# Optimization experiments

Measured on AMD Instinct MI355X. Metric: run time of the kernel, lower is better.

## Reference

```python
import jax, jax.numpy as jnp
import numpy as np

N = 8192
RANK_RATIO = 1.0


def setup_inputs() -> dict:
    key = jax.random.key(0)
    k1, k2, k3 = jax.random.split(key, 3)
    logit = jax.random.normal(k1, (N, 1), dtype=jnp.float32)
    status = jax.random.randint(k2, (N,), 0, 2).astype(jnp.float32)  # event indicator in {0,1}
    time = jax.random.uniform(k3, (N,), dtype=jnp.float32) * 10.0    # survival times
    status_time = jnp.stack([status, time], axis=1)  # [N, 2]
    return {"logit": logit, "status_time": status_time}


def reference(logit, status_time):
    status = status_time[:, 0]
    time = status_time[:, 1]
    lg = -logit.squeeze()  # [N]

    # Comparable pair (i, j): time[i] < time[j] and status[i] == 1.
    # i is the 'low' index (shorter, uncensored time), j is the 'high' index.
    mask = (time[:, None] < time[None, :]) & (status[:, None] == 1.0)  # [N, N]
    # rank term: relu(1 - lg[high] + lg[low])^2 over comparable pairs
    hinge = jnp.maximum(1.0 - lg[None, :] + lg[:, None], 0.0)
    sq = hinge * hinge
    n_pairs = jnp.maximum(jnp.sum(mask), 1)  # mean over selected pairs
    rank_loss = jnp.sum(jnp.where(mask, sq, 0.0)) / n_pairs.astype(sq.dtype)

    uncensor_part = time - lg
    censor_part = jnp.maximum(uncensor_part, 0.0)
    reg_term = (1.0 - status) * censor_part + status * uncensor_part
    reg_loss = jnp.mean(reg_term * reg_term)

    return RANK_RATIO * rank_loss + (1.0 - RANK_RATIO) * reg_loss
```

## Files before the change

kernel.cpp:

```cpp
#include <hip/hip_runtime.h>


typedef float f32x2 __attribute__((ext_vector_type(2)));

constexpr int N_   = 8192;
constexpr int BLK  = 256;
constexpr int R    = 4;
constexpr int JPB  = BLK * R;
constexpr int NJB  = N_ / JPB;
constexpr int ICH  = 32;
constexpr int NIC  = N_ / ICH;
constexpr int GRID = NJB * NIC;

__global__ __launch_bounds__(BLK) void svm_partial(
        const float* __restrict__ logit,
        const float* __restrict__ st,
        float* __restrict__ psum,
        int*   __restrict__ pcnt) {
    __shared__ float2 ci_s[ICH];

    const int jb = blockIdx.x & (NJB - 1);
    const int ic = blockIdx.x / NJB;
    const int j0 = jb * JPB + (int)threadIdx.x * R;

    const float4 lj4 = *(const float4*)(logit + j0);
    const float4 sa  = *(const float4*)(st + 2 * j0);
    const float4 sb  = *(const float4*)(st + 2 * j0 + 4);
    const f32x2 nljpA = { -(1.0f + lj4.x), -(1.0f + lj4.y) };
    const f32x2 nljpB = { -(1.0f + lj4.z), -(1.0f + lj4.w) };
    const float tj0 = sa.y, tj1 = sa.w, tj2 = sb.y, tj3 = sb.w;

    const int i0 = ic * ICH;
    if (threadIdx.x < ICH) {
        const int    i  = i0 + (int)threadIdx.x;
        const float  li = logit[i];
        const float2 sv = *(const float2*)(st + 2 * i);
        const float  te = (sv.x == 1.0f) ? sv.y : 1e30f;
        ci_s[threadIdx.x] = make_float2(li, te);
    }
    __syncthreads();

    f32x2 sA = {0.f, 0.f}, sB = {0.f, 0.f};
    int cnt = 0;
    #pragma unroll 8
    for (int k = 0; k < ICH; ++k) {
        const float2 ct = ci_s[k];
        const float  li = ct.x, te = ct.y;
        const f32x2  li2 = { li, li };
        f32x2 xA = li2 + nljpA;
        f32x2 xB = li2 + nljpB;
        float h0 = fminf(xA.x, 0.f);
        float h1 = fminf(xA.y, 0.f);
        float h2 = fminf(xB.x, 0.f);
        float h3 = fminf(xB.y, 0.f);
        const bool m0 = te < tj0;
        const bool m1 = te < tj1;
        const bool m2 = te < tj2;
        const bool m3 = te < tj3;
        f32x2 hmA = { m0 ? h0 : 0.f, m1 ? h1 : 0.f };
        f32x2 hmB = { m2 ? h2 : 0.f, m3 ? h3 : 0.f };
        sA += hmA * hmA;
        sB += hmB * hmB;
        cnt += (int)__popcll(__ballot(m0));
        cnt += (int)__popcll(__ballot(m1));
        cnt += (int)__popcll(__ballot(m2));
        cnt += (int)__popcll(__ballot(m3));
    }

    float sum = (sA.x + sA.y) + (sB.x + sB.y);
    for (int off = 32; off > 0; off >>= 1)
        sum += __shfl_down(sum, off, 64);

    __shared__ float wsum[BLK / 64];
    __shared__ int   wcnt[BLK / 64];
    const int lane = threadIdx.x & 63;
    const int wid  = threadIdx.x >> 6;
    if (lane == 0) { wsum[wid] = sum; wcnt[wid] = cnt; }
    __syncthreads();
    if (threadIdx.x == 0) {
        psum[blockIdx.x] = (wsum[0] + wsum[1]) + (wsum[2] + wsum[3]);
        pcnt[blockIdx.x] =  wcnt[0] + wcnt[1] + wcnt[2] + wcnt[3];
    }
}

__global__ __launch_bounds__(BLK) void svm_final(
        const float* __restrict__ psum,
        const int* __restrict__ pcnt,
        float* __restrict__ out) {
    float s = 0.f;
    int   c = 0;
    for (int t = (int)threadIdx.x; t < GRID; t += BLK) {
        s += psum[t];
        c += pcnt[t];
    }
    for (int off = 32; off > 0; off >>= 1) {
        s += __shfl_down(s, off, 64);
        c += __shfl_down(c, off, 64);
    }
    __shared__ float wsum[BLK / 64];
    __shared__ int   wcnt[BLK / 64];
    const int lane = threadIdx.x & 63;
    const int wid  = threadIdx.x >> 6;
    if (lane == 0) { wsum[wid] = s; wcnt[wid] = c; }
    __syncthreads();
    if (threadIdx.x == 0) {
        const float S = (wsum[0] + wsum[1]) + (wsum[2] + wsum[3]);
        const int   C =  wcnt[0] + wcnt[1] + wcnt[2] + wcnt[3];
        out[0] = S / (float)(C > 0 ? C : 1);
    }
}

extern "C" void kernel_launch(void* const* d_in, const int* in_sizes, int n_in,
                              void* d_out, int out_size, void* d_ws, size_t ws_size,
                              hipStream_t stream) {
    const float* logit = (const float*)d_in[0];
    const float* st    = (const float*)d_in[1];

    float* psum = (float*)d_ws;
    int*   pcnt = (int*)((char*)d_ws + GRID * 4);

    svm_partial<<<GRID, BLK, 0, stream>>>(logit, st, psum, pcnt);
    svm_final<<<1, BLK, 0, stream>>>(psum, pcnt, (float*)d_out);
}
```

Measured before the change: 19.09 us.

## Fuse final reduction into partial kernel via last-block atomic counters

Merges the two-kernel reduction into a single kernel. Each block publishes a packed (sum,count) pair, and the last block of each group of 32, chosen by an atomic counter, reduces that group. The last group then produces the final output. The i-chunk size is doubled to halve the grid. This removes a second kernel launch and its dependency gap, at the cost of atomics and counters that are never reset but rely on modular wraparound across calls.

```diff
diff --git a/kernel.cpp b/kernel.cpp
--- a/kernel.cpp
+++ b/kernel.cpp
@@ -8,19 +8,28 @@
 constexpr int R    = 4;
 constexpr int JPB  = BLK * R;
 constexpr int NJB  = N_ / JPB;
-constexpr int ICH  = 32;
+constexpr int ICH  = 64;
 constexpr int NIC  = N_ / ICH;
 constexpr int GRID = NJB * NIC;
+constexpr int GSZ  = 32;
+constexpr int NGRP = GRID / GSZ;
 
-__global__ __launch_bounds__(BLK) void svm_partial(
+__global__ __launch_bounds__(BLK) void svm_onepass(
         const float* __restrict__ logit,
         const float* __restrict__ st,
-        float* __restrict__ psum,
-        int*   __restrict__ pcnt) {
+        unsigned long long* __restrict__ pair,
+        unsigned long long* __restrict__ gpair,
+        unsigned int* __restrict__ gcnt,
+        unsigned int* __restrict__ fcnt,
+        float* __restrict__ out) {
     __shared__ float2 ci_s[ICH];
+    __shared__ float  wsum[BLK / 64];
+    __shared__ int    wcnt[BLK / 64];
+    __shared__ bool   lastg_s, lastf_s;
 
     const int jb = blockIdx.x & (NJB - 1);
     const int ic = blockIdx.x / NJB;
+    const int g  = blockIdx.x / GSZ;
     const int j0 = jb * JPB + (int)threadIdx.x * R;
 
     const float4 lj4 = *(const float4*)(logit + j0);
@@ -71,42 +80,71 @@
     for (int off = 32; off > 0; off >>= 1)
         sum += __shfl_down(sum, off, 64);
 
-    __shared__ float wsum[BLK / 64];
-    __shared__ int   wcnt[BLK / 64];
     const int lane = threadIdx.x & 63;
     const int wid  = threadIdx.x >> 6;
     if (lane == 0) { wsum[wid] = sum; wcnt[wid] = cnt; }
     __syncthreads();
     if (threadIdx.x == 0) {
-        psum[blockIdx.x] = (wsum[0] + wsum[1]) + (wsum[2] + wsum[3]);
-        pcnt[blockIdx.x] =  wcnt[0] + wcnt[1] + wcnt[2] + wcnt[3];
+        const float s = (wsum[0] + wsum[1]) + (wsum[2] + wsum[3]);
+        const int   c =  wcnt[0] + wcnt[1] + wcnt[2] + wcnt[3];
+        const unsigned long long p =
+            ((unsigned long long)(unsigned int)c << 32) |
+             (unsigned long long)__float_as_uint(s);
+        __hip_atomic_store(&pair[blockIdx.x], p,
+                           __ATOMIC_RELAXED, __HIP_MEMORY_SCOPE_AGENT);
+        const unsigned int old = __hip_atomic_fetch_add(
+            &gcnt[g], 1u, __ATOMIC_ACQ_REL, __HIP_MEMORY_SCOPE_AGENT);
+        lastg_s = ((old + 1u) & (GSZ - 1u)) == 0u;
     }
-}
+    __syncthreads();
+    if (!lastg_s) return;
 
-__global__ __launch_bounds__(BLK) void svm_final(
-        const float* __restrict__ psum,
-        const int* __restrict__ pcnt,
-        float* __restrict__ out) {
-    float s = 0.f;
-    int   c = 0;
-    for (int t = (int)threadIdx.x; t < GRID; t += BLK) {
-        s += psum[t];
-        c += pcnt[t];
+    {
+        float s = 0.f; int c = 0;
+        if (threadIdx.x < GSZ) {
+            const unsigned long long p = __hip_atomic_load(
+                &pair[g * GSZ + threadIdx.x],
+                __ATOMIC_RELAXED, __HIP_MEMORY_SCOPE_AGENT);
+            s = __uint_as_float((unsigned int)p);
+            c = (int)(unsigned int)(p >> 32);
+        }
+        if (threadIdx.x < 64) {
+            for (int off = 16; off > 0; off >>= 1) {
+                s += __shfl_down(s, off, 64);
+                c += __shfl_down(c, off, 64);
+            }
+            if (threadIdx.x == 0) {
+                const unsigned long long p =
+                    ((unsigned long long)(unsigned int)c << 32) |
+                     (unsigned long long)__float_as_uint(s);
+                __hip_atomic_store(&gpair[g], p,
+                                   __ATOMIC_RELAXED, __HIP_MEMORY_SCOPE_AGENT);
+                const unsigned int old2 = __hip_atomic_fetch_add(
+                    fcnt, 1u, __ATOMIC_ACQ_REL, __HIP_MEMORY_SCOPE_AGENT);
+                lastf_s = ((old2 + 1u) & (NGRP - 1u)) == 0u;
+            }
+        }
     }
-    for (int off = 32; off > 0; off >>= 1) {
-        s += __shfl_down(s, off, 64);
-        c += __shfl_down(c, off, 64);
-    }
-    __shared__ float wsum[BLK / 64];
-    __shared__ int   wcnt[BLK / 64];
-    const int lane = threadIdx.x & 63;
-    const int wid  = threadIdx.x >> 6;
-    if (lane == 0) { wsum[wid] = s; wcnt[wid] = c; }
     __syncthreads();
-    if (threadIdx.x == 0) {
-        const float S = (wsum[0] + wsum[1]) + (wsum[2] + wsum[3]);
-        const int   C =  wcnt[0] + wcnt[1] + wcnt[2] + wcnt[3];
-        out[0] = S / (float)(C > 0 ? C : 1);
+    if (!lastf_s) return;
+
+    {
+        float s = 0.f; int c = 0;
+        if (threadIdx.x < NGRP) {
+            const unsigned long long p = __hip_atomic_load(
+                &gpair[threadIdx.x],
+                __ATOMIC_RELAXED, __HIP_MEMORY_SCOPE_AGENT);
+            s = __uint_as_float((unsigned int)p);
+            c = (int)(unsigned int)(p >> 32);
+        }
+        if (threadIdx.x < 64) {
+            for (int off = 16; off > 0; off >>= 1) {
+                s += __shfl_down(s, off, 64);
+                c += __shfl_down(c, off, 64);
+            }
+            if (threadIdx.x == 0)
+                out[0] = s / (float)(c > 0 ? c : 1);
+        }
     }
 }
 
@@ -116,9 +154,11 @@
     const float* logit = (const float*)d_in[0];
     const float* st    = (const float*)d_in[1];
 
-    float* psum = (float*)d_ws;
-    int*   pcnt = (int*)((char*)d_ws + GRID * 4);
+    unsigned long long* pair  = (unsigned long long*)d_ws;
+    unsigned long long* gpair = (unsigned long long*)((char*)d_ws + 8192);
+    unsigned int*       gcnt  = (unsigned int*)((char*)d_ws + 8448);
+    unsigned int*       fcnt  = (unsigned int*)((char*)d_ws + 8576);
 
-    svm_partial<<<GRID, BLK, 0, stream>>>(logit, st, psum, pcnt);
-    svm_final<<<1, BLK, 0, stream>>>(psum, pcnt, (float*)d_out);
+    svm_onepass<<<GRID, BLK, 0, stream>>>(logit, st, pair, gpair, gcnt, fcnt,
+                                          (float*)d_out);
 }
```

Measured after the change: 28.60 us. 49.9% more time.

## Compact uncensored i rows via ballot and count pairs per lane

Applied to the files above, without the earlier changes.

The i-chunk grows to 64, and only rows with status==1 are compacted into shared memory using a wave ballot and prefix popcount. The inner loop then runs over just those rows, which skips about half of the pair work. Per-iteration ballot/popcount counting is replaced by per-lane integer counters reduced once with shuffles. Because the loop trip count is now data-dependent, unrolling is partial, and the larger chunk halves the grid size.

```diff
diff --git a/kernel.cpp b/kernel.cpp
--- a/kernel.cpp
+++ b/kernel.cpp
@@ -8,7 +8,7 @@
 constexpr int R    = 4;
 constexpr int JPB  = BLK * R;
 constexpr int NJB  = N_ / JPB;
-constexpr int ICH  = 32;
+constexpr int ICH  = 64;
 constexpr int NIC  = N_ / ICH;
 constexpr int GRID = NJB * NIC;
 
@@ -18,6 +18,7 @@
         float* __restrict__ psum,
         int*   __restrict__ pcnt) {
     __shared__ float2 ci_s[ICH];
+    __shared__ int    total_s;
 
     const int jb = blockIdx.x & (NJB - 1);
     const int ic = blockIdx.x / NJB;
@@ -30,20 +31,23 @@
     const f32x2 nljpB = { -(1.0f + lj4.z), -(1.0f + lj4.w) };
     const float tj0 = sa.y, tj1 = sa.w, tj2 = sb.y, tj3 = sb.w;
 
-    const int i0 = ic * ICH;
-    if (threadIdx.x < ICH) {
-        const int    i  = i0 + (int)threadIdx.x;
-        const float  li = logit[i];
-        const float2 sv = *(const float2*)(st + 2 * i);
-        const float  te = (sv.x == 1.0f) ? sv.y : 1e30f;
-        ci_s[threadIdx.x] = make_float2(li, te);
+    if (threadIdx.x < 64) {
+        const int    i    = ic * ICH + (int)threadIdx.x;
+        const float  li   = logit[i];
+        const float2 sv   = *(const float2*)(st + 2 * i);
+        const bool   keep = (sv.x == 1.0f);
+        const unsigned long long mk = __ballot(keep);
+        const int pos = (int)__popcll(mk & ((1ull << threadIdx.x) - 1ull));
+        if (keep) ci_s[pos] = make_float2(li, sv.y);
+        if (threadIdx.x == 0) total_s = (int)__popcll(mk);
     }
     __syncthreads();
+    const int total = total_s;
 
     f32x2 sA = {0.f, 0.f}, sB = {0.f, 0.f};
-    int cnt = 0;
-    #pragma unroll 8
-    for (int k = 0; k < ICH; ++k) {
+    int c0 = 0, c1 = 0, c2 = 0, c3 = 0;
+    #pragma unroll 4
+    for (int k = 0; k < total; ++k) {
         const float2 ct = ci_s[k];
         const float  li = ct.x, te = ct.y;
         const f32x2  li2 = { li, li };
@@ -61,15 +65,18 @@
         f32x2 hmB = { m2 ? h2 : 0.f, m3 ? h3 : 0.f };
         sA += hmA * hmA;
         sB += hmB * hmB;
-        cnt += (int)__popcll(__ballot(m0));
-        cnt += (int)__popcll(__ballot(m1));
-        cnt += (int)__popcll(__ballot(m2));
-        cnt += (int)__popcll(__ballot(m3));
+        c0 += (int)m0;
+        c1 += (int)m1;
+        c2 += (int)m2;
+        c3 += (int)m3;
     }
 
     float sum = (sA.x + sA.y) + (sB.x + sB.y);
-    for (int off = 32; off > 0; off >>= 1)
+    int   cnt = (c0 + c1) + (c2 + c3);
+    for (int off = 32; off > 0; off >>= 1) {
         sum += __shfl_down(sum, off, 64);
+        cnt += __shfl_down(cnt, off, 64);
+    }
 
     __shared__ float wsum[BLK / 64];
     __shared__ int   wcnt[BLK / 64];
```

Result: faster. 16.63 us (-12.9%).
